# Performance work log

Hardware: AMD Instinct MI355X
Metric: run time of the kernel (lower is better)

## Reference

```python
import jax, jax.numpy as jnp
import numpy as np

Z = 20000      # batch (e.g., graph nodes)
U = 128        # segment multiplicity ('u' mode)
S = 8          # segments per operand (same for all 4 operands here)
P = 64         # number of paths


def setup_inputs() -> dict:
    key = jax.random.key(0)
    k0, k1, k2, kc, ki = jax.random.split(key, 5)
    x0 = jax.random.normal(k0, (Z, S * U), dtype=jnp.float32)
    x1 = jax.random.normal(k1, (Z, S * U), dtype=jnp.float32)
    x2 = jax.random.normal(k2, (Z, S * U), dtype=jnp.float32)
    path_coefficients = jax.random.normal(kc, (P,), dtype=jnp.float32)
    # each path picks one segment index per operand (op0, op1, op2, output)
    path_indices = jax.random.randint(ki, (P, 4), 0, S, dtype=jnp.int32)
    return {"x0": x0, "x1": x1, "x2": x2,
            "path_coefficients": path_coefficients,
            "path_indices": path_indices}


def reference(x0, x1, x2, path_coefficients, path_indices):
    # Segmented tensor product, channelwise mode 'u,u,u->u':
    # out[z, i3, u] += sum_p c[p] * x0[z, i0[p], u] * x1[z, i1[p], u] * x2[z, i2[p], u]
    x0s = x0.reshape(Z, S, U)
    x1s = x1.reshape(Z, S, U)
    x2s = x2.reshape(Z, S, U)
    i0, i1, i2, i3 = (path_indices[:, 0], path_indices[:, 1],
                      path_indices[:, 2], path_indices[:, 3])
    # gather segments per path: [Z, P, U]
    prod = (x0s[:, i0, :] * x1s[:, i1, :] * x2s[:, i2, :]
            * path_coefficients[None, :, None])
    # scatter-add paths into output segments: [S, Z, U]
    out = jax.ops.segment_sum(jnp.swapaxes(prod, 0, 1), i3, num_segments=S)
    return jnp.swapaxes(out, 0, 1).reshape(Z, S * U)
```

## Files before the change

kernel.cpp:

```cpp
#include <hip/hip_runtime.h>

constexpr int Zn = 20000;
constexpr int Un = 128;
constexpr int Sn = 8;
constexpr int Pn = 64;
constexpr int ROW = Sn * Un;
constexpr int ZPB = 2;
constexpr int THREADS = 128;

__global__ __launch_bounds__(64) void prep_kernel(const int* __restrict__ pi,
                                                  const float* __restrict__ pc,
                                                  int4* __restrict__ table,
                                                  int* __restrict__ segstart) {
    const int p = threadIdx.x & 63;
    const int i0 = pi[4 * p + 0];
    const int i1 = pi[4 * p + 1];
    const int i2 = pi[4 * p + 2];
    const int i3 = pi[4 * p + 3];
    const float w = pc[p];
    const unsigned long long below = (1ull << p) - 1ull;

    int base = 0, slot = 0;
#pragma unroll
    for (int s = 0; s < Sn; ++s) {
        unsigned long long m = __ballot(i3 == s);
        if (i3 == s) slot = base + __popcll(m & below);
        if (p == 0) segstart[s] = base;
        base += __popcll(m);
    }
    if (p == 0) segstart[Sn] = base;

    table[slot] = make_int4(i0 * Un,
                            ZPB * ROW + i1 * Un,
                            2 * ZPB * ROW + i2 * Un,
                            __float_as_int(w));
}

__global__ __launch_bounds__(THREADS, 3) void tp_kernel(
        const float* __restrict__ x0,
        const float* __restrict__ x1,
        const float* __restrict__ x2,
        const int4* __restrict__ table,
        const int* __restrict__ segstart,
        float* __restrict__ out) {
    __shared__ __align__(16) float lds[3 * ZPB * ROW];
    const int tid = threadIdx.x;
    const int zblk = blockIdx.x * ZPB;

#pragma unroll
    for (int t = 0; t < 3; ++t) {
        const float4* src = (const float4*)(t == 0 ? x0 : (t == 1 ? x1 : x2));
        float4* dst = (float4*)lds + t * (ZPB * ROW / 4);
#pragma unroll
        for (int i = 0; i < (ZPB * ROW / 4) / THREADS; ++i) {
            int local = i * THREADS + tid;
            int z = local >> 8;
            int r = local & 255;
            dst[local] = src[(size_t)(zblk + z) * (ROW / 4) + r];
        }
    }
    __syncthreads();

    int ss[Sn + 1];
#pragma unroll
    for (int i = 0; i <= Sn; ++i) ss[i] = segstart[i];

    const int lane = tid & 63;
    const int wave = tid >> 6;
    const int zloc = lane >> 5;
    const int u4   = lane & 31;
    const float* zb = lds + zloc * ROW;
    float* orow = out + (size_t)(zblk + zloc) * ROW;

#pragma unroll
    for (int s = wave * (Sn / 2); s < (wave + 1) * (Sn / 2); ++s) {
        float4 acc = make_float4(0.f, 0.f, 0.f, 0.f);
        for (int k = ss[s]; k < ss[s + 1]; ++k) {
            int4 e = table[k];
            const float4 a = *(const float4*)(zb + e.x + u4 * 4);
            const float4 b = *(const float4*)(zb + e.y + u4 * 4);
            const float4 c = *(const float4*)(zb + e.z + u4 * 4);
            const float w = __int_as_float(e.w);
            acc.x += a.x * b.x * c.x * w;
            acc.y += a.y * b.y * c.y * w;
            acc.z += a.z * b.z * c.z * w;
            acc.w += a.w * b.w * c.w * w;
        }
        *(float4*)(orow + s * Un + u4 * 4) = acc;
    }
}

extern "C" void kernel_launch(void* const* d_in, const int* in_sizes, int n_in,
                              void* d_out, int out_size, void* d_ws, size_t ws_size,
                              hipStream_t stream) {
    const float* x0 = (const float*)d_in[0];
    const float* x1 = (const float*)d_in[1];
    const float* x2 = (const float*)d_in[2];
    const float* pc = (const float*)d_in[3];
    const int*   pi = (const int*)d_in[4];
    float* out = (float*)d_out;

    int4* table    = (int4*)d_ws;
    int*  segstart = (int*)((char*)d_ws + Pn * sizeof(int4));

    prep_kernel<<<1, 64, 0, stream>>>(pi, pc, table, segstart);
    tp_kernel<<<Zn / ZPB, THREADS, 0, stream>>>(x0, x1, x2, table, segstart, out);
}
```

Before: 276.5 us.

## Use 4 waves per block, each owning 2 segments in a single merged path loop

Doubles the block to 256 threads so each wave handles two output segments instead of four, and merges both segments' path lists into one loop that routes each product into one of two accumulators using masked weights. Segment bounds are read before the barrier, and the next table entry is prefetched through a wave-uniform index to hide load latency. The merged loop does two FMAs per element per path instead of one. It also assumes the two segments' paths are contiguous in the table, which the prep kernel's sorted layout guarantees.

```diff
diff --git a/kernel.cpp b/kernel.cpp
--- a/kernel.cpp
+++ b/kernel.cpp
@@ -6,7 +6,7 @@
 constexpr int Pn = 64;
 constexpr int ROW = Sn * Un;
 constexpr int ZPB = 2;
-constexpr int THREADS = 128;
+constexpr int THREADS = 256;
 
 __global__ __launch_bounds__(64) void prep_kernel(const int* __restrict__ pi,
                                                   const float* __restrict__ pc,
@@ -36,7 +36,7 @@
                             __float_as_int(w));
 }
 
-__global__ __launch_bounds__(THREADS, 3) void tp_kernel(
+__global__ __launch_bounds__(THREADS, 6) void tp_kernel(
         const float* __restrict__ x0,
         const float* __restrict__ x1,
         const float* __restrict__ x2,
@@ -59,35 +59,55 @@
             dst[local] = src[(size_t)(zblk + z) * (ROW / 4) + r];
         }
     }
-    __syncthreads();
-
-    int ss[Sn + 1];
-#pragma unroll
-    for (int i = 0; i <= Sn; ++i) ss[i] = segstart[i];
 
     const int lane = tid & 63;
     const int wave = tid >> 6;
     const int zloc = lane >> 5;
     const int u4   = lane & 31;
+    const int s0   = wave * 2;
+
+    const int kbeg = segstart[s0];
+    const int kmid = segstart[s0 + 1];
+    const int kend = segstart[s0 + 2];
+
+    __syncthreads();
+
     const float* zb = lds + zloc * ROW;
+    float4 acc0 = make_float4(0.f, 0.f, 0.f, 0.f);
+    float4 acc1 = make_float4(0.f, 0.f, 0.f, 0.f);
+
+    int4 e = table[__builtin_amdgcn_readfirstlane(kbeg < kend ? kbeg : 0)];
+    for (int k = kbeg; k < kend; ++k) {
+        const int kn = (k + 1 < kend) ? k + 1 : k;
+        const int4 en = table[__builtin_amdgcn_readfirstlane(kn)];
+
+        const float4 a = *(const float4*)(zb + e.x + u4 * 4);
+        const float4 b = *(const float4*)(zb + e.y + u4 * 4);
+        const float4 c = *(const float4*)(zb + e.z + u4 * 4);
+        const float w  = __int_as_float(e.w);
+        const float w0 = (k < kmid) ? w : 0.f;
+        const float w1 = (k < kmid) ? 0.f : w;
+
+        float4 p;
+        p.x = a.x * b.x * c.x;
+        p.y = a.y * b.y * c.y;
+        p.z = a.z * b.z * c.z;
+        p.w = a.w * b.w * c.w;
+        acc0.x = fmaf(p.x, w0, acc0.x);
+        acc0.y = fmaf(p.y, w0, acc0.y);
+        acc0.z = fmaf(p.z, w0, acc0.z);
+        acc0.w = fmaf(p.w, w0, acc0.w);
+        acc1.x = fmaf(p.x, w1, acc1.x);
+        acc1.y = fmaf(p.y, w1, acc1.y);
+        acc1.z = fmaf(p.z, w1, acc1.z);
+        acc1.w = fmaf(p.w, w1, acc1.w);
+
+        e = en;
+    }
+
     float* orow = out + (size_t)(zblk + zloc) * ROW;
-
-#pragma unroll
-    for (int s = wave * (Sn / 2); s < (wave + 1) * (Sn / 2); ++s) {
-        float4 acc = make_float4(0.f, 0.f, 0.f, 0.f);
-        for (int k = ss[s]; k < ss[s + 1]; ++k) {
-            int4 e = table[k];
-            const float4 a = *(const float4*)(zb + e.x + u4 * 4);
-            const float4 b = *(const float4*)(zb + e.y + u4 * 4);
-            const float4 c = *(const float4*)(zb + e.z + u4 * 4);
-            const float w = __int_as_float(e.w);
-            acc.x += a.x * b.x * c.x * w;
-            acc.y += a.y * b.y * c.y * w;
-            acc.z += a.z * b.z * c.z * w;
-            acc.w += a.w * b.w * c.w * w;
-        }
-        *(float4*)(orow + s * Un + u4 * 4) = acc;
-    }
+    *(float4*)(orow + s0 * Un + u4 * 4) = acc0;
+    *(float4*)(orow + (s0 + 1) * Un + u4 * 4) = acc1;
 }
 
 extern "C" void kernel_launch(void* const* d_in, const int* in_sizes, int n_in,
```

Result: faster. 260.6 us (-5.7%).

## Persistent double-buffered kernel with async global-to-LDS loads and one segment per wave

Applied to the files above, without the earlier changes.

Turns the one-block-per-row-pair launch into a persistent grid of 768 blocks of 512 threads. Each block loops over row pairs, double-buffering them in LDS with global_load_lds direct copies so the next pair's load overlaps compute on the current one. Each of the 8 waves owns one output segment, the path table is cached in LDS, and the loads for the next path are software-pipelined. The cost is twice the LDS per block and explicit waitcnt and barrier handling, which cap occupancy and add per-iteration synchronization.

```diff
diff --git a/kernel.cpp b/kernel.cpp
--- a/kernel.cpp
+++ b/kernel.cpp
@@ -1,4 +1,5 @@
 #include <hip/hip_runtime.h>
+#include <stdint.h>
 
 constexpr int Zn = 20000;
 constexpr int Un = 128;
@@ -6,7 +7,10 @@
 constexpr int Pn = 64;
 constexpr int ROW = Sn * Un;
 constexpr int ZPB = 2;
-constexpr int THREADS = 128;
+constexpr int NZP = Zn / ZPB;
+constexpr int THREADS = 512;
+constexpr int GRID = 768;
+constexpr int BUFF = 3 * ZPB * ROW;
 
 __global__ __launch_bounds__(64) void prep_kernel(const int* __restrict__ pi,
                                                   const float* __restrict__ pc,
@@ -36,57 +40,89 @@
                             __float_as_int(w));
 }
 
-__global__ __launch_bounds__(THREADS, 3) void tp_kernel(
+__global__ __launch_bounds__(THREADS, 6) void tp_kernel(
         const float* __restrict__ x0,
         const float* __restrict__ x1,
         const float* __restrict__ x2,
         const int4* __restrict__ table,
         const int* __restrict__ segstart,
         float* __restrict__ out) {
-    __shared__ __align__(16) float lds[3 * ZPB * ROW];
-    const int tid = threadIdx.x;
-    const int zblk = blockIdx.x * ZPB;
+    __shared__ __align__(16) float lds[2 * BUFF];
+    __shared__ __align__(16) int4 tbl[Pn];
 
-#pragma unroll
-    for (int t = 0; t < 3; ++t) {
-        const float4* src = (const float4*)(t == 0 ? x0 : (t == 1 ? x1 : x2));
-        float4* dst = (float4*)lds + t * (ZPB * ROW / 4);
-#pragma unroll
-        for (int i = 0; i < (ZPB * ROW / 4) / THREADS; ++i) {
-            int local = i * THREADS + tid;
-            int z = local >> 8;
-            int r = local & 255;
-            dst[local] = src[(size_t)(zblk + z) * (ROW / 4) + r];
-        }
-    }
-    __syncthreads();
-
-    int ss[Sn + 1];
-#pragma unroll
-    for (int i = 0; i <= Sn; ++i) ss[i] = segstart[i];
-
+    const int tid  = threadIdx.x;
     const int lane = tid & 63;
     const int wave = tid >> 6;
     const int zloc = lane >> 5;
     const int u4   = lane & 31;
-    const float* zb = lds + zloc * ROW;
-    float* orow = out + (size_t)(zblk + zloc) * ROW;
 
+    const int kbeg = segstart[wave];
+    const int kend = segstart[wave + 1];
+    if (tid < Pn) tbl[tid] = table[tid];
+
+    const int zs = tid >> 8;
+    const int rs = tid & 255;
+
+    auto ISSUE = [&](int buf, int zp) {
 #pragma unroll
-    for (int s = wave * (Sn / 2); s < (wave + 1) * (Sn / 2); ++s) {
+        for (int t = 0; t < 3; ++t) {
+            const float4* src = (const float4*)(t == 0 ? x0 : (t == 1 ? x1 : x2));
+            const float4* g = src + (size_t)(zp * ZPB + zs) * (ROW / 4) + rs;
+            float* l = lds + buf * BUFF + t * (ZPB * ROW) + tid * 4;
+            __builtin_amdgcn_global_load_lds(
+                (const __attribute__((address_space(1))) void*)g,
+                (__attribute__((address_space(3))) void*)l, 16, 0, 0);
+        }
+    };
+
+    int zp  = blockIdx.x;
+    int cur = 0;
+    ISSUE(0, zp);
+
+    for (;;) {
+        const int zpn = zp + GRID;
+        const bool more = zpn < NZP;
+        if (more) {
+            ISSUE(cur ^ 1, zpn);
+            asm volatile("s_waitcnt vmcnt(3)" ::: "memory");
+        } else {
+            asm volatile("s_waitcnt vmcnt(0)" ::: "memory");
+        }
+        __builtin_amdgcn_s_barrier();
+        asm volatile("" ::: "memory");
+
+        const float* zb = lds + cur * BUFF + zloc * ROW;
         float4 acc = make_float4(0.f, 0.f, 0.f, 0.f);
-        for (int k = ss[s]; k < ss[s + 1]; ++k) {
-            int4 e = table[k];
-            const float4 a = *(const float4*)(zb + e.x + u4 * 4);
-            const float4 b = *(const float4*)(zb + e.y + u4 * 4);
-            const float4 c = *(const float4*)(zb + e.z + u4 * 4);
-            const float w = __int_as_float(e.w);
-            acc.x += a.x * b.x * c.x * w;
-            acc.y += a.y * b.y * c.y * w;
-            acc.z += a.z * b.z * c.z * w;
-            acc.w += a.w * b.w * c.w * w;
+
+        int4 e0 = tbl[kbeg < kend ? kbeg : 0];
+        float4 a0 = *(const float4*)(zb + e0.x + u4 * 4);
+        float4 b0 = *(const float4*)(zb + e0.y + u4 * 4);
+        float4 c0 = *(const float4*)(zb + e0.z + u4 * 4);
+
+        for (int k = kbeg; k < kend; ++k) {
+            const int kn = (k + 1 < kend) ? k + 1 : k;
+            const int4 e1 = tbl[kn];
+            const float4 a1 = *(const float4*)(zb + e1.x + u4 * 4);
+            const float4 b1 = *(const float4*)(zb + e1.y + u4 * 4);
+            const float4 c1 = *(const float4*)(zb + e1.z + u4 * 4);
+
+            const float w = __int_as_float(e0.w);
+            acc.x = fmaf(a0.x * b0.x * c0.x, w, acc.x);
+            acc.y = fmaf(a0.y * b0.y * c0.y, w, acc.y);
+            acc.z = fmaf(a0.z * b0.z * c0.z, w, acc.z);
+            acc.w = fmaf(a0.w * b0.w * c0.w, w, acc.w);
+
+            e0 = e1; a0 = a1; b0 = b1; c0 = c1;
         }
-        *(float4*)(orow + s * Un + u4 * 4) = acc;
+
+        float* orow = out + (size_t)(zp * ZPB + zloc) * ROW;
+        *(float4*)(orow + wave * Un + u4 * 4) = acc;
+
+        asm volatile("" ::: "memory");
+        __builtin_amdgcn_s_barrier();
+        if (!more) break;
+        cur ^= 1;
+        zp = zpn;
     }
 }
 
@@ -104,5 +140,5 @@
     int*  segstart = (int*)((char*)d_ws + Pn * sizeof(int4));
 
     prep_kernel<<<1, 64, 0, stream>>>(pi, pc, table, segstart);
-    tp_kernel<<<Zn / ZPB, THREADS, 0, stream>>>(x0, x1, x2, table, segstart, out);
+    tp_kernel<<<GRID, THREADS, 0, stream>>>(x0, x1, x2, table, segstart, out);
 }
```

Result: faster. 264.2 us (-4.4%).
